# Optimization experiments

Measured on AMD Instinct MI355X. Metric: run time of the kernel, lower is better.

## Reference

```python
import jax, jax.numpy as jnp
import numpy as np

B, I, J, DIN, DOUT = 256, 1152, 10, 8, 16
ROUTING_ITERS = 3


def squash(v):
    # v: [..., D]; squash(v) = (|v|^2 / (1+|v|^2)) * v/|v| = v * |v| / (1+|v|^2)
    l2 = jnp.linalg.norm(v, axis=-1, keepdims=True)
    return v * (l2 / (1.0 + l2 * l2))


def setup_inputs() -> dict:
    key = jax.random.key(0)
    k1, k2 = jax.random.split(key)
    x = jax.random.normal(k1, (B, I, DIN), dtype=jnp.float32)
    # per-(i,j) Linear(DIN -> DOUT, bias=False) weights, stacked: [I, J, DOUT, DIN]
    W = jax.random.normal(k2, (I, J, DOUT, DIN), dtype=jnp.float32) * 0.1
    return {"x": x, "W": W}


def reference(x, W):
    # prediction vectors u[b,i,j,:] = W[i,j] @ x[b,i,:]  -> [B, I, J, DOUT]
    u = jnp.einsum('bid,ijod->bijo', x, W)
    b = jnp.zeros((I, J), dtype=u.dtype)  # routing logits (shared across batch)
    s = None
    for _ in range(ROUTING_ITERS):
        c = jax.nn.softmax(b, axis=-1)              # [I, J]
        s = jnp.einsum('ij,bijd->bjd', c, u)        # coupling-weighted sum over in-caps
        s = squash(s)                               # [B, J, DOUT]
        # agreement: b[i,j] += sum_b <u[b,i,j], s[b,j]>
        b = b + jnp.einsum('bijd,bjd->ij', u, s)
    return s
```

## Files before the change

### kernel.cpp

```cpp
#include <hip/hip_runtime.h>
#include <math.h>

typedef unsigned short ushort_t;
typedef __attribute__((ext_vector_type(8))) __bf16 bf16x8;
typedef __attribute__((ext_vector_type(4))) float floatx4;

#define B_    256
#define I_    1152
#define J_    10
#define DIN_  8
#define DOUT_ 16
#define K_    (I_*DIN_)
#define N_    (J_*DOUT_)
#define KSPLIT 16
#define KCHUNK (K_/KSPLIT)
#define KSTEPS (KCHUNK/32)
#define CHUNK16 2368

static __device__ __forceinline__ ushort_t f2bf(float f) {
    unsigned int u = __float_as_uint(f);
    u += 0x7fffu + ((u >> 16) & 1u);
    return (ushort_t)(u >> 16);
}
static __device__ __forceinline__ float bf2f(ushort_t h) {
    return __uint_as_float(((unsigned int)h) << 16);
}
static __device__ __forceinline__ void ast_f(float* p, float v) {
    __hip_atomic_store(p, v, __ATOMIC_RELAXED, __HIP_MEMORY_SCOPE_AGENT);
}
static __device__ __forceinline__ float ald_f(const float* p) {
    return __hip_atomic_load(p, __ATOMIC_RELAXED, __HIP_MEMORY_SCOPE_AGENT);
}

static __device__ __forceinline__
void ab_epilogue(float* __restrict__ pbuf_it, unsigned int* __restrict__ cnt_it,
                 float* __restrict__ s_out, ushort_t* __restrict__ Sbt_hi,
                 ushort_t* __restrict__ Sbt_lo, const floatx4* part, int* last_s,
                 int tile, int kb, int mb, int nt, int tid, int it)
{
    const int row = tid >> 4;
    const int o   = tid & 15;
    const int lane_c = ((row >> 2) << 4) | o;
    const int reg    = row & 3;
    float v = part[0 * 64 + lane_c][reg] + part[1 * 64 + lane_c][reg]
            + part[2 * 64 + lane_c][reg] + part[3 * 64 + lane_c][reg];
    ast_f(pbuf_it + (size_t)(tile * 8 + kb) * 256 + row * 16 + o, v);
    __syncthreads();
    if (tid == 0)
        *last_s = (atomicAdd(cnt_it + tile, 1u) == 7u);
    __syncthreads();
    if (!*last_s) return;

    const float* pb = pbuf_it + (size_t)tile * 8 * 256 + row * 16 + o;
    float vv = 0.f;
    #pragma unroll
    for (int u = 0; u < 8; ++u)
        vv += ald_f(pb + u * 256);
    float sq = vv * vv;
    #pragma unroll
    for (int off = 1; off < 16; off <<= 1)
        sq += __shfl_xor(sq, off, 16);
    float l2 = sqrtf(sq);
    float val = vv * (l2 / (1.f + sq));
    const int b  = mb * 16 + row;
    const int jo = nt * 16 + o;
    if (it == 2) {
        s_out[(size_t)b * N_ + jo] = val;
    } else {
        ushort_t hi = f2bf(val);
        Sbt_hi[(size_t)jo * B_ + b] = hi;
        Sbt_lo[(size_t)jo * B_ + b] = f2bf(val - bf2f(hi));
    }
}

__global__ __launch_bounds__(256)
void d1_kernel(const float* __restrict__ x, const float* __restrict__ W,
               ushort_t* __restrict__ xPk, float* __restrict__ wPk,
               float* __restrict__ pbuf, unsigned int* __restrict__ cnt,
               float* __restrict__ s_out,
               ushort_t* __restrict__ Sbt_hi, ushort_t* __restrict__ Sbt_lo)
{
    const int blk = blockIdx.x;
    const int tid = threadIdx.x;

    if (blk >= 1280) {
        if (blk < 2432) {
            const int gid = (blk - 1280) * 256 + tid;
            const int f   = gid * 8;
            const int row = f / K_;
            const int kk  = f - row * K_;
            const int kc  = kk / KCHUNK;
            const int t   = kk - kc * KCHUNK;
            const int s   = t >> 5;
            const int q   = (t & 31) >> 3;
            const int mb  = row >> 4, r = row & 15;
            const float* src = x + (size_t)f;
            bf16x8 h8, l8;
            #pragma unroll
            for (int e = 0; e < 8; ++e) {
                float v = src[e];
                __bf16 h = (__bf16)v;
                h8[e] = h;
                l8[e] = (__bf16)(v - (float)h);
            }
            bf16x8* dst = (bf16x8*)xPk + (size_t)(mb * 16 + kc) * CHUNK16 + s * 128 + q * 16 + r;
            dst[0]  = h8;
            dst[64] = l8;
        } else {
            const int gid = (blk - 2432) * 256 + tid;
            const int f   = gid * 4;
            const int i   = f / 1280;
            const int rem = f - i * 1280;
            const int no  = rem >> 3;
            const int p   = (rem >> 2) & 1;
            const int nt  = no >> 4, r = no & 15;
            const int kc  = i / 72;
            const int m   = i - kc * 72;
            const int s   = m >> 2, q = m & 3;
            float4 v = *(const float4*)(W + (size_t)f);
            ((float4*)wPk)[(size_t)(nt * 16 + kc) * CHUNK16 + (s * 2 + p) * 64 + q * 16 + r] = v;
        }
        return;
    }

    const int kb    = blk & 7;
    const int tile  = blk >> 3;
    const int mb    = tile & 15;
    const int nt    = tile >> 4;
    const int lane  = tid & 63;
    const int w     = tid >> 6;
    const int kc    = kb * 2 + (w >> 1);
    const int sbase = (w & 1) * 9;

    __shared__ floatx4 part[4 * 64];
    __shared__ int     last_s;

    {
        const int r = lane & 15, q = lane >> 4;
        const float* ap = x + (size_t)(mb * 16 + r) * K_ + kc * KCHUNK + 8 * q + sbase * 32;
        const float* wp = W + (((size_t)(kc * 72 + q) * J_ + nt) * DOUT_ + r) * DIN_;
        const size_t wstep = (size_t)4 * J_ * DOUT_ * DIN_;
        const float* wps = wp + sbase * wstep;
        floatx4 acc = {0.f, 0.f, 0.f, 0.f};

        float4 bxa0[2], bxa1[2], bw0[2], bw1[2];
        #pragma unroll
        for (int s = 0; s < 2; ++s) {
            bxa0[s] = *(const float4*)(ap + s * 32);
            bxa1[s] = *(const float4*)(ap + s * 32 + 4);
            bw0[s]  = *(const float4*)(wps + s * wstep);
            bw1[s]  = *(const float4*)(wps + s * wstep + 4);
        }
        #pragma unroll
        for (int s = 0; s < 9; ++s) {
            float4 xa0 = bxa0[s & 1], xa1 = bxa1[s & 1];
            float4 w0  = bw0[s & 1],  w1  = bw1[s & 1];
            if (s + 2 < 9) {
                bxa0[s & 1] = *(const float4*)(ap + (s + 2) * 32);
                bxa1[s & 1] = *(const float4*)(ap + (s + 2) * 32 + 4);
                bw0[s & 1]  = *(const float4*)(wps + (s + 2) * wstep);
                bw1[s & 1]  = *(const float4*)(wps + (s + 2) * wstep + 4);
            }
            const float cs = 0.1f;
            float xv[8]  = {xa0.x, xa0.y, xa0.z, xa0.w, xa1.x, xa1.y, xa1.z, xa1.w};
            float wvv[8] = {w0.x, w0.y, w0.z, w0.w, w1.x, w1.y, w1.z, w1.w};
            bf16x8 ah, al, bh, bl;
            #pragma unroll
            for (int e = 0; e < 8; ++e) {
                float xe = xv[e];
                __bf16 h = (__bf16)xe;
                ah[e] = h;
                al[e] = (__bf16)(xe - (float)h);
                float pe = wvv[e] * cs;
                __bf16 g = (__bf16)pe;
                bh[e] = g;
                bl[e] = (__bf16)(pe - (float)g);
            }
            acc = __builtin_amdgcn_mfma_f32_16x16x32_bf16(ah, bh, acc, 0, 0, 0);
            acc = __builtin_amdgcn_mfma_f32_16x16x32_bf16(al, bh, acc, 0, 0, 0);
            acc = __builtin_amdgcn_mfma_f32_16x16x32_bf16(ah, bl, acc, 0, 0, 0);
        }
        part[w * 64 + lane] = acc;
    }
    __syncthreads();
    ab_epilogue(pbuf, cnt, s_out, Sbt_hi, Sbt_lo, part, &last_s,
                tile, kb, mb, nt, tid, 0);
}

__global__ __launch_bounds__(256)
void gemm_s_ab_kernel(const ushort_t* __restrict__ xPk, const float* __restrict__ wPk,
                      const float* __restrict__ blog,
                      float* __restrict__ pbuf, unsigned int* __restrict__ cnt,
                      float* __restrict__ s_out,
                      ushort_t* __restrict__ Sbt_hi, ushort_t* __restrict__ Sbt_lo,
                      const int iter)
{
    const int tid   = threadIdx.x;
    const int blk   = blockIdx.x;
    const int kb    = blk & 7;
    const int tile  = blk >> 3;
    const int mb    = tile & 15;
    const int nt    = tile >> 4;
    const int lane  = tid & 63;
    const int w     = tid >> 6;
    const int kc    = kb * 2 + (w >> 1);
    const int shalf = w & 1;

    __shared__ float   c_lds[144];
    __shared__ floatx4 part[4 * 64];
    __shared__ int     last_s;

    {
        for (int r2 = tid; r2 < 144; r2 += 256) {
            const float* br = blog + (size_t)(kb * 144 + r2) * J_;
            float bv[J_];
            float mx = -1e30f;
            #pragma unroll
            for (int j = 0; j < J_; ++j) { bv[j] = br[j]; mx = fmaxf(mx, bv[j]); }
            float sum = 0.f;
            #pragma unroll
            for (int j = 0; j < J_; ++j) { bv[j] = __expf(bv[j] - mx); sum += bv[j]; }
            c_lds[r2] = bv[nt] / sum;
        }
        __syncthreads();
    }

    {
        const int q = lane >> 4;
        const int sbase = shalf * 9;
        const bf16x8* xp = (const bf16x8*)xPk + (size_t)(mb * 16 + kc) * CHUNK16
                           + sbase * 128 + lane;
        const float4* wp = (const float4*)wPk + (size_t)(nt * 16 + kc) * CHUNK16
                           + sbase * 128 + lane;
        floatx4 acc = {0.f, 0.f, 0.f, 0.f};

        bf16x8 rah[2], ral[2];
        float4 rw0[2], rw1[2];
        #pragma unroll
        for (int s = 0; s < 2; ++s) {
            rah[s] = xp[s * 128];
            ral[s] = xp[s * 128 + 64];
            rw0[s] = wp[s * 128];
            rw1[s] = wp[s * 128 + 64];
        }
        #pragma unroll
        for (int s = 0; s < 9; ++s) {
            bf16x8 ah = rah[s & 1], al = ral[s & 1];
            float4 w0 = rw0[s & 1], w1 = rw1[s & 1];
            if (s + 2 < 9) {
                rah[s & 1] = xp[(s + 2) * 128];
                ral[s & 1] = xp[(s + 2) * 128 + 64];
                rw0[s & 1] = wp[(s + 2) * 128];
                rw1[s & 1] = wp[(s + 2) * 128 + 64];
            }
            float cs = c_lds[(w >> 1) * 72 + 4 * (sbase + s) + q];
            float wvv[8] = {w0.x, w0.y, w0.z, w0.w, w1.x, w1.y, w1.z, w1.w};
            bf16x8 bh, bl;
            #pragma unroll
            for (int e = 0; e < 8; ++e) {
                float pe = wvv[e] * cs;
                __bf16 g = (__bf16)pe;
                bh[e] = g;
                bl[e] = (__bf16)(pe - (float)g);
            }
            acc = __builtin_amdgcn_mfma_f32_16x16x32_bf16(ah, bh, acc, 0, 0, 0);
            acc = __builtin_amdgcn_mfma_f32_16x16x32_bf16(al, bh, acc, 0, 0, 0);
            acc = __builtin_amdgcn_mfma_f32_16x16x32_bf16(ah, bl, acc, 0, 0, 0);
        }
        part[w * 64 + lane] = acc;
    }
    __syncthreads();
    ab_epilogue(pbuf, cnt, s_out, Sbt_hi, Sbt_lo, part, &last_s,
                tile, kb, mb, nt, tid, iter);
}

__global__ __launch_bounds__(256)
void gemm_bupd_kernel(const float* __restrict__ x,
                      const ushort_t* __restrict__ Sbt_hi, const ushort_t* __restrict__ Sbt_lo,
                      const float* __restrict__ W, float* __restrict__ blog,
                      const int first)
{
    int wv   = (blockIdx.x & 7) * 360 + (blockIdx.x >> 3) * 4 + (threadIdx.x >> 6);
    int lane = threadIdx.x & 63;
    int mt = wv / 5;
    int jp = wv - mt * 5;
    int j0 = jp * 2, j1 = jp * 2 + 1;
    int r = lane & 15, q = lane >> 4;
    const float* xp = x + (size_t)(8 * q) * K_ + (mt * 16 + r);
    size_t b0off = (size_t)(j0 * 16 + r) * B_ + 8 * q;
    size_t b1off = (size_t)(j1 * 16 + r) * B_ + 8 * q;
    floatx4 acc0 = {0.f, 0.f, 0.f, 0.f};
    floatx4 acc1 = {0.f, 0.f, 0.f, 0.f};

    float xcur[8], xnxt[8];
    #pragma unroll
    for (int e = 0; e < 8; ++e) xcur[e] = xp[(size_t)e * K_];
    #pragma unroll
    for (int s = 0; s < B_ / 32; ++s) {
        if (s + 1 < B_ / 32) {
            #pragma unroll
            for (int e = 0; e < 8; ++e)
                xnxt[e] = xp[(size_t)((s + 1) * 32 + e) * K_];
        }
        bf16x8 ah, al;
        #pragma unroll
        for (int e = 0; e < 8; ++e) {
            float v = xcur[e];
            __bf16 h = (__bf16)v;
            ah[e] = h;
            al[e] = (__bf16)(v - (float)h);
        }
        bf16x8 bh0 = *(const bf16x8*)(Sbt_hi + b0off + s * 32);
        bf16x8 bl0 = *(const bf16x8*)(Sbt_lo + b0off + s * 32);
        bf16x8 bh1 = *(const bf16x8*)(Sbt_hi + b1off + s * 32);
        bf16x8 bl1 = *(const bf16x8*)(Sbt_lo + b1off + s * 32);
        acc0 = __builtin_amdgcn_mfma_f32_16x16x32_bf16(ah, bh0, acc0, 0, 0, 0);
        acc0 = __builtin_amdgcn_mfma_f32_16x16x32_bf16(al, bh0, acc0, 0, 0, 0);
        acc0 = __builtin_amdgcn_mfma_f32_16x16x32_bf16(ah, bl0, acc0, 0, 0, 0);
        acc1 = __builtin_amdgcn_mfma_f32_16x16x32_bf16(ah, bh1, acc1, 0, 0, 0);
        acc1 = __builtin_amdgcn_mfma_f32_16x16x32_bf16(al, bh1, acc1, 0, 0, 0);
        acc1 = __builtin_amdgcn_mfma_f32_16x16x32_bf16(ah, bl1, acc1, 0, 0, 0);
        #pragma unroll
        for (int e = 0; e < 8; ++e) xcur[e] = xnxt[e];
    }
    int i  = mt * 2 + (q >> 1);
    int d0 = (q & 1) * 4;
    int o  = lane & 15;
    int iw = mt * 2 + (lane >> 5);
    {
        const float4 w4 = *(const float4*)(W + ((((size_t)i * J_ + j0) * DOUT_ + o) * DIN_ + d0));
        float val = acc0[0] * w4.x + acc0[1] * w4.y + acc0[2] * w4.z + acc0[3] * w4.w;
        #pragma unroll
        for (int off = 1; off < 32; off <<= 1)
            val += __shfl_xor(val, off, 32);
        if ((lane & 31) == 0) {
            float* dst = blog + (size_t)iw * J_ + j0;
            if (first) *dst = val; else *dst += val;
        }
    }
    {
        const float4 w4 = *(const float4*)(W + ((((size_t)i * J_ + j1) * DOUT_ + o) * DIN_ + d0));
        float val = acc1[0] * w4.x + acc1[1] * w4.y + acc1[2] * w4.z + acc1[3] * w4.w;
        #pragma unroll
        for (int off = 1; off < 32; off <<= 1)
            val += __shfl_xor(val, off, 32);
        if ((lane & 31) == 0) {
            float* dst = blog + (size_t)iw * J_ + j1;
            if (first) *dst = val; else *dst += val;
        }
    }
}

extern "C" void kernel_launch(void* const* d_in, const int* in_sizes, int n_in,
                              void* d_out, int out_size, void* d_ws, size_t ws_size,
                              hipStream_t stream)
{
    const float* x = (const float*)d_in[0];
    const float* W = (const float*)d_in[1];
    float* s_out = (float*)d_out;

    char* ws = (char*)d_ws;
    ushort_t*     Sbt_hi = (ushort_t*)(ws);
    ushort_t*     Sbt_lo = (ushort_t*)(ws + 81920);
    float*        blog   = (float*)   (ws + 163840);
    float*        pbuf   = (float*)   (ws + 262144);
    ushort_t*     xPk    = (ushort_t*)(ws + 4194304);
    float*        wPk    = (float*)   (ws + 13893632);
    unsigned int* cnt    = (unsigned int*)(ws + 19955712);

    (void)hipMemsetAsync(ws + 19955712, 0, 1920, stream);

    d1_kernel<<<3872, 256, 0, stream>>>(x, W, xPk, wPk,
                                        pbuf, cnt, s_out, Sbt_hi, Sbt_lo);
    gemm_bupd_kernel<<<720, 256, 0, stream>>>(x, Sbt_hi, Sbt_lo, W, blog, 1);
    gemm_s_ab_kernel<<<1280, 256, 0, stream>>>(xPk, wPk, blog,
                                               pbuf + 327680, cnt + 160,
                                               s_out, Sbt_hi, Sbt_lo, 1);
    gemm_bupd_kernel<<<720, 256, 0, stream>>>(x, Sbt_hi, Sbt_lo, W, blog, 0);
    gemm_s_ab_kernel<<<1280, 256, 0, stream>>>(xPk, wPk, blog,
                                               pbuf + 655360, cnt + 320,
                                               s_out, Sbt_hi, Sbt_lo, 2);
}
```

Baseline: 140.6 us.

## Split K-split reduction into separate squash kernels and pre-transpose x to bf16

Replaces the last-block-done atomic counter epilogue, which used agent-scope atomics, a memset and extra barriers, with plain partial-sum stores followed by a small reduce_squash kernel per iteration. Adds a transposed hi/lo bf16 copy of x, built in extra d1 blocks through LDS, so the b-update GEMM loads packed bf16 vectors. This replaces strided fp32 gathers and per-iteration bf16 splitting. The cost is three extra kernel launches and more workspace traffic for the transposed x copy.

```diff
diff --git a/kernel.cpp b/kernel.cpp
--- a/kernel.cpp
+++ b/kernel.cpp
@@ -3,6 +3,7 @@
 
 typedef unsigned short ushort_t;
 typedef __attribute__((ext_vector_type(8))) __bf16 bf16x8;
+typedef __attribute__((ext_vector_type(8))) ushort_t ushort8;
 typedef __attribute__((ext_vector_type(4))) float floatx4;
 
 #define B_    256
@@ -25,63 +26,17 @@
 static __device__ __forceinline__ float bf2f(ushort_t h) {
     return __uint_as_float(((unsigned int)h) << 16);
 }
-static __device__ __forceinline__ void ast_f(float* p, float v) {
-    __hip_atomic_store(p, v, __ATOMIC_RELAXED, __HIP_MEMORY_SCOPE_AGENT);
-}
-static __device__ __forceinline__ float ald_f(const float* p) {
-    return __hip_atomic_load(p, __ATOMIC_RELAXED, __HIP_MEMORY_SCOPE_AGENT);
-}
-
-static __device__ __forceinline__
-void ab_epilogue(float* __restrict__ pbuf_it, unsigned int* __restrict__ cnt_it,
-                 float* __restrict__ s_out, ushort_t* __restrict__ Sbt_hi,
-                 ushort_t* __restrict__ Sbt_lo, const floatx4* part, int* last_s,
-                 int tile, int kb, int mb, int nt, int tid, int it)
-{
-    const int row = tid >> 4;
-    const int o   = tid & 15;
-    const int lane_c = ((row >> 2) << 4) | o;
-    const int reg    = row & 3;
-    float v = part[0 * 64 + lane_c][reg] + part[1 * 64 + lane_c][reg]
-            + part[2 * 64 + lane_c][reg] + part[3 * 64 + lane_c][reg];
-    ast_f(pbuf_it + (size_t)(tile * 8 + kb) * 256 + row * 16 + o, v);
-    __syncthreads();
-    if (tid == 0)
-        *last_s = (atomicAdd(cnt_it + tile, 1u) == 7u);
-    __syncthreads();
-    if (!*last_s) return;
-
-    const float* pb = pbuf_it + (size_t)tile * 8 * 256 + row * 16 + o;
-    float vv = 0.f;
-    #pragma unroll
-    for (int u = 0; u < 8; ++u)
-        vv += ald_f(pb + u * 256);
-    float sq = vv * vv;
-    #pragma unroll
-    for (int off = 1; off < 16; off <<= 1)
-        sq += __shfl_xor(sq, off, 16);
-    float l2 = sqrtf(sq);
-    float val = vv * (l2 / (1.f + sq));
-    const int b  = mb * 16 + row;
-    const int jo = nt * 16 + o;
-    if (it == 2) {
-        s_out[(size_t)b * N_ + jo] = val;
-    } else {
-        ushort_t hi = f2bf(val);
-        Sbt_hi[(size_t)jo * B_ + b] = hi;
-        Sbt_lo[(size_t)jo * B_ + b] = f2bf(val - bf2f(hi));
-    }
-}
 
 __global__ __launch_bounds__(256)
 void d1_kernel(const float* __restrict__ x, const float* __restrict__ W,
                ushort_t* __restrict__ xPk, float* __restrict__ wPk,
-               float* __restrict__ pbuf, unsigned int* __restrict__ cnt,
-               float* __restrict__ s_out,
-               ushort_t* __restrict__ Sbt_hi, ushort_t* __restrict__ Sbt_lo)
+               ushort_t* __restrict__ xTh, ushort_t* __restrict__ xTl,
+               float* __restrict__ pbuf)
 {
     const int blk = blockIdx.x;
     const int tid = threadIdx.x;
+
+    __shared__ __align__(16) char smem[16384];
 
     if (blk >= 1280) {
         if (blk < 2432) {
@@ -106,7 +61,9 @@
             bf16x8* dst = (bf16x8*)xPk + (size_t)(mb * 16 + kc) * CHUNK16 + s * 128 + q * 16 + r;
             dst[0]  = h8;
             dst[64] = l8;
-        } else {
+            return;
+        }
+        if (blk < 3872) {
             const int gid = (blk - 2432) * 256 + tid;
             const int f   = gid * 4;
             const int i   = f / 1280;
@@ -119,10 +76,44 @@
             const int s   = m >> 2, q = m & 3;
             float4 v = *(const float4*)(W + (size_t)f);
             ((float4*)wPk)[(size_t)(nt * 16 + kc) * CHUNK16 + (s * 2 + p) * 64 + q * 16 + r] = v;
-        }
-        return;
-    }
-
+            return;
+        }
+        {
+            ushort_t* lh = (ushort_t*)smem;
+            ushort_t* ll = (ushort_t*)(smem + 8192);
+            const int m0 = (blk - 3872) * 16;
+            const int b  = tid;
+            const float* src = x + (size_t)b * K_ + m0;
+            #pragma unroll
+            for (int v = 0; v < 4; ++v) {
+                float4 f4 = *(const float4*)(src + v * 4);
+                float vv[4] = {f4.x, f4.y, f4.z, f4.w};
+                #pragma unroll
+                for (int e = 0; e < 4; ++e) {
+                    const int ml = v * 4 + e;
+                    float val = vv[e];
+                    __bf16 h = (__bf16)val;
+                    lh[ml * 256 + b] = (ushort_t)__builtin_bit_cast(unsigned short, h);
+                    ll[ml * 256 + b] = (ushort_t)__builtin_bit_cast(unsigned short,
+                                        (__bf16)(val - (float)h));
+                }
+            }
+            __syncthreads();
+            #pragma unroll
+            for (int v = 0; v < 2; ++v) {
+                const int idx = tid + v * 256;
+                const int mm  = idx >> 5;
+                const int b8  = idx & 31;
+                *(ushort8*)(xTh + (size_t)(m0 + mm) * B_ + b8 * 8) =
+                    *(const ushort8*)(lh + mm * 256 + b8 * 8);
+                *(ushort8*)(xTl + (size_t)(m0 + mm) * B_ + b8 * 8) =
+                    *(const ushort8*)(ll + mm * 256 + b8 * 8);
+            }
+            return;
+        }
+    }
+
+    floatx4* part = (floatx4*)smem;
     const int kb    = blk & 7;
     const int tile  = blk >> 3;
     const int mb    = tile & 15;
@@ -131,9 +122,6 @@
     const int w     = tid >> 6;
     const int kc    = kb * 2 + (w >> 1);
     const int sbase = (w & 1) * 9;
-
-    __shared__ floatx4 part[4 * 64];
-    __shared__ int     last_s;
 
     {
         const int r = lane & 15, q = lane >> 4;
@@ -183,17 +171,20 @@
         part[w * 64 + lane] = acc;
     }
     __syncthreads();
-    ab_epilogue(pbuf, cnt, s_out, Sbt_hi, Sbt_lo, part, &last_s,
-                tile, kb, mb, nt, tid, 0);
+
+    const int row = tid >> 4;
+    const int o   = tid & 15;
+    const int lane_c = ((row >> 2) << 4) | o;
+    const int reg    = row & 3;
+    float v = part[0 * 64 + lane_c][reg] + part[1 * 64 + lane_c][reg]
+            + part[2 * 64 + lane_c][reg] + part[3 * 64 + lane_c][reg];
+    pbuf[(size_t)blk * 256 + row * 16 + o] = v;
 }
 
 __global__ __launch_bounds__(256)
-void gemm_s_ab_kernel(const ushort_t* __restrict__ xPk, const float* __restrict__ wPk,
-                      const float* __restrict__ blog,
-                      float* __restrict__ pbuf, unsigned int* __restrict__ cnt,
-                      float* __restrict__ s_out,
-                      ushort_t* __restrict__ Sbt_hi, ushort_t* __restrict__ Sbt_lo,
-                      const int iter)
+void gemm_s_part_kernel(const ushort_t* __restrict__ xPk, const float* __restrict__ wPk,
+                        const float* __restrict__ blog,
+                        float* __restrict__ pbuf, const int iter)
 {
     const int tid   = threadIdx.x;
     const int blk   = blockIdx.x;
@@ -208,7 +199,6 @@
 
     __shared__ float   c_lds[144];
     __shared__ floatx4 part[4 * 64];
-    __shared__ int     last_s;
 
     {
         for (int r2 = tid; r2 < 144; r2 += 256) {
@@ -270,12 +260,53 @@
         part[w * 64 + lane] = acc;
     }
     __syncthreads();
-    ab_epilogue(pbuf, cnt, s_out, Sbt_hi, Sbt_lo, part, &last_s,
-                tile, kb, mb, nt, tid, iter);
+
+    const int row = tid >> 4;
+    const int o   = tid & 15;
+    const int lane_c = ((row >> 2) << 4) | o;
+    const int reg    = row & 3;
+    float v = part[0 * 64 + lane_c][reg] + part[1 * 64 + lane_c][reg]
+            + part[2 * 64 + lane_c][reg] + part[3 * 64 + lane_c][reg];
+    pbuf[(size_t)blk * 256 + row * 16 + o] = v;
 }
 
 __global__ __launch_bounds__(256)
-void gemm_bupd_kernel(const float* __restrict__ x,
+void reduce_squash_kernel(const float* __restrict__ pbuf, float* __restrict__ s_out,
+                          ushort_t* __restrict__ Sbt_hi, ushort_t* __restrict__ Sbt_lo,
+                          const int iter)
+{
+    const int tile = blockIdx.x;
+    const int mb   = tile & 15;
+    const int nt   = tile >> 4;
+    const int t    = threadIdx.x;
+    const int row  = t >> 4;
+    const int o    = t & 15;
+
+    const float* pb = pbuf + (size_t)tile * 8 * 256 + row * 16 + o;
+    float v = 0.f;
+    #pragma unroll
+    for (int u = 0; u < 8; ++u)
+        v += pb[u * 256];
+
+    float sq = v * v;
+    #pragma unroll
+    for (int off = 1; off < 16; off <<= 1)
+        sq += __shfl_xor(sq, off, 16);
+    float l2 = sqrtf(sq);
+    float val = v * (l2 / (1.f + sq));
+    const int b  = mb * 16 + row;
+    const int jo = nt * 16 + o;
+    if (iter == 2) {
+        s_out[(size_t)b * N_ + jo] = val;
+    } else {
+        ushort_t hi = f2bf(val);
+        Sbt_hi[(size_t)jo * B_ + b] = hi;
+        Sbt_lo[(size_t)jo * B_ + b] = f2bf(val - bf2f(hi));
+    }
+}
+
+__global__ __launch_bounds__(256)
+void gemm_bupd_kernel(const ushort_t* __restrict__ xTh, const ushort_t* __restrict__ xTl,
                       const ushort_t* __restrict__ Sbt_hi, const ushort_t* __restrict__ Sbt_lo,
                       const float* __restrict__ W, float* __restrict__ blog,
                       const int first)
@@ -286,30 +317,17 @@
     int jp = wv - mt * 5;
     int j0 = jp * 2, j1 = jp * 2 + 1;
     int r = lane & 15, q = lane >> 4;
-    const float* xp = x + (size_t)(8 * q) * K_ + (mt * 16 + r);
+    const ushort_t* xh = xTh + (size_t)(mt * 16 + r) * B_ + 8 * q;
+    const ushort_t* xl = xTl + (size_t)(mt * 16 + r) * B_ + 8 * q;
     size_t b0off = (size_t)(j0 * 16 + r) * B_ + 8 * q;
     size_t b1off = (size_t)(j1 * 16 + r) * B_ + 8 * q;
     floatx4 acc0 = {0.f, 0.f, 0.f, 0.f};
     floatx4 acc1 = {0.f, 0.f, 0.f, 0.f};
 
-    float xcur[8], xnxt[8];
-    #pragma unroll
-    for (int e = 0; e < 8; ++e) xcur[e] = xp[(size_t)e * K_];
     #pragma unroll
     for (int s = 0; s < B_ / 32; ++s) {
-        if (s + 1 < B_ / 32) {
-            #pragma unroll
-            for (int e = 0; e < 8; ++e)
-                xnxt[e] = xp[(size_t)((s + 1) * 32 + e) * K_];
-        }
-        bf16x8 ah, al;
-        #pragma unroll
-        for (int e = 0; e < 8; ++e) {
-            float v = xcur[e];
-            __bf16 h = (__bf16)v;
-            ah[e] = h;
-            al[e] = (__bf16)(v - (float)h);
-        }
+        bf16x8 ah = *(const bf16x8*)(xh + s * 32);
+        bf16x8 al = *(const bf16x8*)(xl + s * 32);
         bf16x8 bh0 = *(const bf16x8*)(Sbt_hi + b0off + s * 32);
         bf16x8 bl0 = *(const bf16x8*)(Sbt_lo + b0off + s * 32);
         bf16x8 bh1 = *(const bf16x8*)(Sbt_hi + b1off + s * 32);
@@ -320,8 +338,6 @@
         acc1 = __builtin_amdgcn_mfma_f32_16x16x32_bf16(ah, bh1, acc1, 0, 0, 0);
         acc1 = __builtin_amdgcn_mfma_f32_16x16x32_bf16(al, bh1, acc1, 0, 0, 0);
         acc1 = __builtin_amdgcn_mfma_f32_16x16x32_bf16(ah, bl1, acc1, 0, 0, 0);
-        #pragma unroll
-        for (int e = 0; e < 8; ++e) xcur[e] = xnxt[e];
     }
     int i  = mt * 2 + (q >> 1);
     int d0 = (q & 1) * 4;
@@ -360,24 +376,21 @@
     float* s_out = (float*)d_out;
 
     char* ws = (char*)d_ws;
-    ushort_t*     Sbt_hi = (ushort_t*)(ws);
-    ushort_t*     Sbt_lo = (ushort_t*)(ws + 81920);
-    float*        blog   = (float*)   (ws + 163840);
-    float*        pbuf   = (float*)   (ws + 262144);
-    ushort_t*     xPk    = (ushort_t*)(ws + 4194304);
-    float*        wPk    = (float*)   (ws + 13893632);
-    unsigned int* cnt    = (unsigned int*)(ws + 19955712);
-
-    (void)hipMemsetAsync(ws + 19955712, 0, 1920, stream);
-
-    d1_kernel<<<3872, 256, 0, stream>>>(x, W, xPk, wPk,
-                                        pbuf, cnt, s_out, Sbt_hi, Sbt_lo);
-    gemm_bupd_kernel<<<720, 256, 0, stream>>>(x, Sbt_hi, Sbt_lo, W, blog, 1);
-    gemm_s_ab_kernel<<<1280, 256, 0, stream>>>(xPk, wPk, blog,
-                                               pbuf + 327680, cnt + 160,
-                                               s_out, Sbt_hi, Sbt_lo, 1);
-    gemm_bupd_kernel<<<720, 256, 0, stream>>>(x, Sbt_hi, Sbt_lo, W, blog, 0);
-    gemm_s_ab_kernel<<<1280, 256, 0, stream>>>(xPk, wPk, blog,
-                                               pbuf + 655360, cnt + 320,
-                                               s_out, Sbt_hi, Sbt_lo, 2);
-}
+    ushort_t* Sbt_hi = (ushort_t*)(ws);
+    ushort_t* Sbt_lo = (ushort_t*)(ws + 81920);
+    float*    blog   = (float*)   (ws + 163840);
+    float*    pbuf   = (float*)   (ws + 262144);
+    ushort_t* xPk    = (ushort_t*)(ws + 1572864);
+    float*    wPk    = (float*)   (ws + 11272192);
+    ushort_t* xTh    = (ushort_t*)(ws + 17334272);
+    ushort_t* xTl    = (ushort_t*)(ws + 22052864);
+
+    d1_kernel<<<4448, 256, 0, stream>>>(x, W, xPk, wPk, xTh, xTl, pbuf);
+    reduce_squash_kernel<<<160, 256, 0, stream>>>(pbuf, s_out, Sbt_hi, Sbt_lo, 0);
+    gemm_bupd_kernel<<<720, 256, 0, stream>>>(xTh, xTl, Sbt_hi, Sbt_lo, W, blog, 1);
+    gemm_s_part_kernel<<<1280, 256, 0, stream>>>(xPk, wPk, blog, pbuf, 1);
+    reduce_squash_kernel<<<160, 256, 0, stream>>>(pbuf, s_out, Sbt_hi, Sbt_lo, 1);
+    gemm_bupd_kernel<<<720, 256, 0, stream>>>(xTh, xTl, Sbt_hi, Sbt_lo, W, blog, 0);
+    gemm_s_part_kernel<<<1280, 256, 0, stream>>>(xPk, wPk, blog, pbuf, 2);
+    reduce_squash_kernel<<<160, 256, 0, stream>>>(pbuf, s_out, Sbt_hi, Sbt_lo, 2);
+}
```

Result: slower. 151.5 us (+7.8%).
